# Kernel tuning notes

Hardware: AMD Instinct MI355X
Metric: run time of the kernel (lower is better)

Reference implementation:

```python
import jax, jax.numpy as jnp
import numpy as np

N = 100000
E = 1_600_000
IN_DIM = 128
HIDDEN = 128


def spmm(row, col, vals, H):
    # y[r] = sum_{edges e with row[e]==r} vals[e] * H[col[e]]
    msgs = vals[:, None] * H[col]          # [E, hidden] gather + scale
    return jax.ops.segment_sum(msgs, row, num_segments=H.shape[0])


def setup_inputs() -> dict:
    key = jax.random.key(0)
    ks = jax.random.split(key, 10)
    X = jax.random.normal(ks[0], (N, IN_DIM), dtype=jnp.float32)
    row = jax.random.randint(ks[1], (E,), 0, N, dtype=jnp.int32)
    col = jax.random.randint(ks[2], (E,), 0, N, dtype=jnp.int32)
    vals = jax.random.uniform(ks[3], (E,), dtype=jnp.float32)
    s_in = 1.0 / np.sqrt(IN_DIM)
    s_h = 1.0 / np.sqrt(HIDDEN)
    W_in = jax.random.normal(ks[4], (IN_DIM, HIDDEN), dtype=jnp.float32) * s_in
    b_in = jax.random.normal(ks[5], (HIDDEN,), dtype=jnp.float32) * s_in
    W_mp1 = jax.random.normal(ks[6], (HIDDEN, HIDDEN), dtype=jnp.float32) * s_h
    W_mp2 = jax.random.normal(ks[7], (HIDDEN, HIDDEN), dtype=jnp.float32) * s_h
    W_out = jax.random.normal(ks[8], (HIDDEN, 1), dtype=jnp.float32) * s_h
    b_out = jax.random.normal(ks[9], (1,), dtype=jnp.float32) * s_h
    return {"X": X, "row": row, "col": col, "vals": vals,
            "W_in": W_in, "b_in": b_in, "W_mp1": W_mp1, "W_mp2": W_mp2,
            "W_out": W_out, "b_out": b_out}


def reference(X, row, col, vals, W_in, b_in, W_mp1, W_mp2, W_out, b_out):
    H = jax.nn.relu(X @ W_in + b_in)          # [N, hidden]
    AH = spmm(row, col, vals, H)              # 1-hop propagation
    A2H = spmm(row, col, vals, AH)            # 2-hop propagation
    H2 = jax.nn.relu(AH @ W_mp1 + A2H @ W_mp2)
    return H2 @ W_out + b_out                 # [N, 1]
```

## Files before the change

### kernel.cpp

```cpp
#include <hip/hip_runtime.h>

#define N_NODES 100000
#define N_EDGES 1600000
#define NBUCK 391
#define NCHUNK 256
#define CHUNK 6250
#define LROW 136
#define DCAP 5120

typedef float f32x4 __attribute__((ext_vector_type(4)));
typedef _Float16 f16x8 __attribute__((ext_vector_type(8)));
typedef _Float16 h16x2 __attribute__((ext_vector_type(2)));

__device__ __forceinline__ unsigned f2h_bits(float f) {
    union { _Float16 h; unsigned short s; } c;
    c.h = (_Float16)f;
    return c.s;
}
__device__ __forceinline__ h16x2 u2h(unsigned u) {
    union { unsigned u; h16x2 h; } c;
    c.u = u;
    return c.h;
}
__device__ __forceinline__ unsigned pk16lo(unsigned hi, unsigned lo) {
    return __builtin_amdgcn_perm(hi, lo, 0x05040100u);
}
__device__ __forceinline__ unsigned pk16hi(unsigned hi, unsigned lo) {
    return __builtin_amdgcn_perm(hi, lo, 0x07060302u);
}
__device__ __forceinline__ float fdot2(h16x2 a, h16x2 b, float c) {
#if __has_builtin(__builtin_amdgcn_fdot2)
    return __builtin_amdgcn_fdot2(a, b, c, false);
#else
    return c + (float)a[0] * (float)b[0] + (float)a[1] * (float)b[1];
#endif
}

__device__ __forceinline__ f16x8 pack_h8(float4 a, float4 b) {
    f16x8 r;
    r[0] = (_Float16)a.x; r[1] = (_Float16)a.y;
    r[2] = (_Float16)a.z; r[3] = (_Float16)a.w;
    r[4] = (_Float16)b.x; r[5] = (_Float16)b.y;
    r[6] = (_Float16)b.z; r[7] = (_Float16)b.w;
    return r;
}


__global__ __launch_bounds__(256) void k_prep(const int* __restrict__ row,
                                              int* __restrict__ hmat,
                                              const float* __restrict__ Wa,
                                              const float* __restrict__ Wb,
                                              const float* __restrict__ Wc,
                                              unsigned short* __restrict__ Wta,
                                              unsigned short* __restrict__ Wtb,
                                              unsigned short* __restrict__ Wtc) {
    if (blockIdx.x < NCHUNK) {
        __shared__ int h[NBUCK];
        for (int i = threadIdx.x; i < NBUCK; i += 256) h[i] = 0;
        __syncthreads();
        int s = blockIdx.x * CHUNK, e = s + CHUNK;
        for (int i = s + threadIdx.x; i < e; i += 256)
            atomicAdd(&h[row[i] >> 8], 1);
        __syncthreads();
        for (int b = threadIdx.x; b < NBUCK; b += 256)
            hmat[blockIdx.x * NBUCK + b] = h[b];
    } else {
        int t = (blockIdx.x - NCHUNK) * 256 + threadIdx.x;
        int which = t >> 14;
        int i = t & 16383;
        int n = i & 127, k = i >> 7;
        const float* W = which == 0 ? Wa : which == 1 ? Wb : Wc;
        unsigned short* Wt = which == 0 ? Wta : which == 1 ? Wtb : Wtc;
        Wt[n * 128 + k] = (unsigned short)f2h_bits(W[k * 128 + n]);
    }
}

__global__ __launch_bounds__(512) void k_colscanB(const int* __restrict__ hmat,
                                                  int* __restrict__ bases,
                                                  int* __restrict__ bstart) {
    __shared__ int s[512];
    int b = blockIdx.x, t = threadIdx.x;
    if (b < NBUCK) {
        int v = (t < NCHUNK) ? hmat[t * NBUCK + b] : 0;
        s[t] = v;
        __syncthreads();
        for (int off = 1; off < 512; off <<= 1) {
            int x = (t >= off) ? s[t - off] : 0;
            __syncthreads();
            s[t] += x;
            __syncthreads();
        }
        if (t < NCHUNK) bases[t * NBUCK + b] = s[t] - v;
    } else {
        int v = 0;
        if (t < NBUCK) {
            for (int blk = 0; blk < NCHUNK; blk++) v += hmat[blk * NBUCK + t];
        }
        s[t] = v;
        __syncthreads();
        for (int off = 1; off < 512; off <<= 1) {
            int x = (t >= off) ? s[t - off] : 0;
            __syncthreads();
            s[t] += x;
            __syncthreads();
        }
        if (t < NBUCK) bstart[t] = s[t] - v;
        if (t == NBUCK) bstart[NBUCK] = N_EDGES;
    }
}

__global__ __launch_bounds__(256) void k_binC_gemm(const int* __restrict__ row,
                                                   const int* __restrict__ col,
                                                   const float* __restrict__ vals,
                                                   const int* __restrict__ bstart,
                                                   const int* __restrict__ bases,
                                                   int2* __restrict__ grouped,
                                                   const float* __restrict__ X,
                                                   const unsigned short* __restrict__ Wt,
                                                   const float* __restrict__ bvec,
                                                   unsigned short* __restrict__ H) {
    __shared__ __align__(16) char smraw[64 * LROW * 2];
    if (blockIdx.x < NCHUNK) {
        int* cnt = (int*)smraw;
        int* basl = (int*)(smraw + 1600);
        for (int i = threadIdx.x; i < NBUCK; i += 256) {
            cnt[i] = 0;
            basl[i] = bstart[i] + bases[blockIdx.x * NBUCK + i];
        }
        __syncthreads();
        int s = blockIdx.x * CHUNK, e = s + CHUNK;
        for (int i = s + threadIdx.x; i < e; i += 256) {
            int r = row[i];
            int b = r >> 8;
            int rank = atomicAdd(&cnt[b], 1);
            int pos = basl[b] + rank;
            unsigned hv = f2h_bits(vals[i]);
            grouped[pos] = make_int2(col[i], ((r & 255) << 14) | hv);
        }
    } else {
        unsigned short* lds = (unsigned short*)smraw;
        int tid = threadIdx.x;
        int lane = tid & 63, wv = tid >> 6;
        int quad = lane >> 4, c16 = lane & 15;

        f16x8 wf[2][4];
        float bb[2];
#pragma unroll
        for (int nt = 0; nt < 2; nt++) {
            int ng = wv * 2 + nt;
            bb[nt] = bvec[ng * 16 + c16];
#pragma unroll
            for (int kc = 0; kc < 4; kc++)
                wf[nt][kc] = *(const f16x8*)&Wt[(ng * 16 + c16) * 128 + kc * 32 + quad * 8];
        }

        int tilebase = (blockIdx.x - NCHUNK) * 64;
        const float4* Xg = (const float4*)X;
#pragma unroll
        for (int i = 0; i < 4; i++) {
            int c = tid + i * 256;
            int r = c >> 4, o = c & 15;
            int grow = tilebase + r;
            float4 f0 = make_float4(0.f, 0.f, 0.f, 0.f), f1 = f0;
            if (grow < N_NODES) {
                f0 = Xg[(size_t)grow * 32 + o * 2];
                f1 = Xg[(size_t)grow * 32 + o * 2 + 1];
            }
            *(f16x8*)&lds[r * LROW + o * 8] = pack_h8(f0, f1);
        }
        __syncthreads();

        f32x4 acc[4][2] = {};
#pragma unroll
        for (int t4 = 0; t4 < 4; t4++) {
#pragma unroll
            for (int kc = 0; kc < 4; kc++) {
                f16x8 af = *(const f16x8*)&lds[(t4 * 16 + c16) * LROW + kc * 32 + quad * 8];
#pragma unroll
                for (int nt = 0; nt < 2; nt++)
                    acc[t4][nt] = __builtin_amdgcn_mfma_f32_16x16x32_f16(af, wf[nt][kc],
                                                                        acc[t4][nt], 0, 0, 0);
            }
        }
        __syncthreads();

#pragma unroll
        for (int t4 = 0; t4 < 4; t4++)
#pragma unroll
            for (int nt = 0; nt < 2; nt++) {
                int ncol = (wv * 2 + nt) * 16 + c16;
#pragma unroll
                for (int r = 0; r < 4; r++) {
                    float v = fmaxf(acc[t4][nt][r] + bb[nt], 0.f);
                    lds[(t4 * 16 + quad * 4 + r) * LROW + ncol] = (unsigned short)f2h_bits(v);
                }
            }
        __syncthreads();
#pragma unroll
        for (int i = 0; i < 4; i++) {
            int c = tid + i * 256;
            int r = c >> 4, o = c & 15;
            int grow = tilebase + r;
            if (grow < N_NODES)
                *(uint4*)&H[(size_t)grow * 128 + o * 8] = *(const uint4*)&lds[r * LROW + o * 8];
        }
    }
}

__global__ __launch_bounds__(512) void k_binD(const int2* __restrict__ grouped,
                                              const int* __restrict__ bstart,
                                              unsigned* __restrict__ evf,
                                              int* __restrict__ row_ptr) {
    __shared__ int h[256], sc[256], cur[256];
    __shared__ int2 ebuf[DCAP];
    int b = blockIdx.x, t = threadIdx.x;
    int s0 = bstart[b], e0 = bstart[b + 1];
    int n = e0 - s0;
    bool inlds = (n <= DCAP);
    if (t < 256) h[t] = 0;
    __syncthreads();
    if (inlds) {
        for (int i = t; i < n; i += 512) ebuf[i] = grouped[s0 + i];
        __syncthreads();
        for (int i = t; i < n; i += 512)
            atomicAdd(&h[(ebuf[i].y >> 14) & 255], 1);
    } else {
        for (int i = s0 + t; i < e0; i += 512)
            atomicAdd(&h[(grouped[i].y >> 14) & 255], 1);
    }
    __syncthreads();
    int v = 0;
    if (t < 256) {
        v = h[t];
        sc[t] = v;
    }
    __syncthreads();
    for (int off = 1; off < 256; off <<= 1) {
        int x = (t >= off && t < 256) ? sc[t - off] : 0;
        __syncthreads();
        if (t < 256) sc[t] += x;
        __syncthreads();
    }
    if (t < 256) {
        int excl = sc[t] - v;
        cur[t] = excl;
        int grow = b * 256 + t;
        if (grow <= N_NODES) row_ptr[grow] = s0 + excl;
    }
    __syncthreads();
    if (inlds) {
        for (int i = t; i < n; i += 512) {
            int2 g = ebuf[i];
            int rl = (g.y >> 14) & 255;
            int p = atomicAdd(&cur[rl], 1);
            evf[s0 + p] = ((unsigned)g.x << 14) | (unsigned)(g.y & 0x3fff);
        }
    } else {
        for (int i = s0 + t; i < e0; i += 512) {
            int2 g = grouped[i];
            int rl = (g.y >> 14) & 255;
            int p = atomicAdd(&cur[rl], 1);
            evf[s0 + p] = ((unsigned)g.x << 14) | (unsigned)(g.y & 0x3fff);
        }
    }
}

__global__ __launch_bounds__(256) void k_spmm(const int* __restrict__ rp,
                                              const unsigned* __restrict__ evf,
                                              const unsigned* __restrict__ Hin,
                                              unsigned* __restrict__ Ho) {
    int tid = threadIdx.x;
    int lane = tid & 63;
    int q = lane >> 4, l16 = lane & 15;
    int wid = (blockIdx.x * 256 + tid) >> 6;
    int r0 = wid * 4 + q;
    int s = rp[r0];
    int e = rp[r0 + 1];
    float a0 = 0.f, a1 = 0.f, a2 = 0.f, a3 = 0.f;
    float a4 = 0.f, a5 = 0.f, a6 = 0.f, a7 = 0.f;
    for (int base = s; base < e; base += 16) {
        int cnt = e - base;
        if (cnt > 16) cnt = 16;
        unsigned ev = evf[base + (l16 < cnt ? l16 : cnt - 1)];
        for (int i = 0; i < cnt; i += 4) {
            int i1 = i + 1, i2 = i + 2, i3 = i + 3;
            unsigned u0 = __shfl(ev, (q << 4) + i, 64);
            unsigned u1 = __shfl(ev, (q << 4) + (i1 < cnt ? i1 : cnt - 1), 64);
            unsigned u2 = __shfl(ev, (q << 4) + (i2 < cnt ? i2 : cnt - 1), 64);
            unsigned u3 = __shfl(ev, (q << 4) + (i3 < cnt ? i3 : cnt - 1), 64);
            const uint4 h0 = *(const uint4*)&Hin[(size_t)(u0 >> 14) * 64 + l16 * 4];
            const uint4 h1 = *(const uint4*)&Hin[(size_t)(u1 >> 14) * 64 + l16 * 4];
            const uint4 h2 = *(const uint4*)&Hin[(size_t)(u2 >> 14) * 64 + l16 * 4];
            const uint4 h3 = *(const uint4*)&Hin[(size_t)(u3 >> 14) * 64 + l16 * 4];
            unsigned m0 = u0 & 0x3fffu;
            unsigned m1 = (i1 < cnt) ? (u1 & 0x3fffu) : 0u;
            unsigned m2 = (i2 < cnt) ? (u2 & 0x3fffu) : 0u;
            unsigned m3 = (i3 < cnt) ? (u3 & 0x3fffu) : 0u;
            h16x2 v01 = u2h(pk16lo(m1, m0));
            h16x2 v23 = u2h(pk16lo(m3, m2));
            a0 = fdot2(v01, u2h(pk16lo(h1.x, h0.x)), a0);
            a0 = fdot2(v23, u2h(pk16lo(h3.x, h2.x)), a0);
            a1 = fdot2(v01, u2h(pk16hi(h1.x, h0.x)), a1);
            a1 = fdot2(v23, u2h(pk16hi(h3.x, h2.x)), a1);
            a2 = fdot2(v01, u2h(pk16lo(h1.y, h0.y)), a2);
            a2 = fdot2(v23, u2h(pk16lo(h3.y, h2.y)), a2);
            a3 = fdot2(v01, u2h(pk16hi(h1.y, h0.y)), a3);
            a3 = fdot2(v23, u2h(pk16hi(h3.y, h2.y)), a3);
            a4 = fdot2(v01, u2h(pk16lo(h1.z, h0.z)), a4);
            a4 = fdot2(v23, u2h(pk16lo(h3.z, h2.z)), a4);
            a5 = fdot2(v01, u2h(pk16hi(h1.z, h0.z)), a5);
            a5 = fdot2(v23, u2h(pk16hi(h3.z, h2.z)), a5);
            a6 = fdot2(v01, u2h(pk16lo(h1.w, h0.w)), a6);
            a6 = fdot2(v23, u2h(pk16lo(h3.w, h2.w)), a6);
            a7 = fdot2(v01, u2h(pk16hi(h1.w, h0.w)), a7);
            a7 = fdot2(v23, u2h(pk16hi(h3.w, h2.w)), a7);
        }
    }
    uint4 p;
    p.x = (f2h_bits(a1) << 16) | f2h_bits(a0);
    p.y = (f2h_bits(a3) << 16) | f2h_bits(a2);
    p.z = (f2h_bits(a5) << 16) | f2h_bits(a4);
    p.w = (f2h_bits(a7) << 16) | f2h_bits(a6);
    *(uint4*)&Ho[(size_t)r0 * 64 + l16 * 4] = p;
}

__global__ __launch_bounds__(256) void k_gemm_out(const unsigned short* __restrict__ AH,
                                                  const unsigned short* __restrict__ A2H,
                                                  const unsigned short* __restrict__ Wt1,
                                                  const unsigned short* __restrict__ Wt2,
                                                  const float* __restrict__ Wout,
                                                  const float* __restrict__ bout,
                                                  float* __restrict__ out) {
    __shared__ unsigned short lds[2][64 * LROW];
    __shared__ float part[4][64];
    int tid = threadIdx.x;
    int lane = tid & 63, wv = tid >> 6;
    int quad = lane >> 4, c16 = lane & 15;

    f16x8 w1f[2][4], w2f[2][4];
    float wo[2];
#pragma unroll
    for (int nt = 0; nt < 2; nt++) {
        int ng = wv * 2 + nt;
        wo[nt] = Wout[ng * 16 + c16];
#pragma unroll
        for (int kc = 0; kc < 4; kc++) {
            w1f[nt][kc] = *(const f16x8*)&Wt1[(ng * 16 + c16) * 128 + kc * 32 + quad * 8];
            w2f[nt][kc] = *(const f16x8*)&Wt2[(ng * 16 + c16) * 128 + kc * 32 + quad * 8];
        }
    }
    float bo = bout[0];

    int tilebase = blockIdx.x * 64;
    const uint4* Ag = (const uint4*)(AH + (size_t)tilebase * 128);
    const uint4* Bg = (const uint4*)(A2H + (size_t)tilebase * 128);
#pragma unroll
    for (int i = 0; i < 4; i++) {
        int c = tid + i * 256;
        int r = c >> 4, o = c & 15;
        *(uint4*)&lds[0][r * LROW + o * 8] = Ag[c];
        *(uint4*)&lds[1][r * LROW + o * 8] = Bg[c];
    }
    __syncthreads();

    f32x4 acc[4][2] = {};
#pragma unroll
    for (int t4 = 0; t4 < 4; t4++) {
#pragma unroll
        for (int kc = 0; kc < 4; kc++) {
            f16x8 afA = *(const f16x8*)&lds[0][(t4 * 16 + c16) * LROW + kc * 32 + quad * 8];
            f16x8 afB = *(const f16x8*)&lds[1][(t4 * 16 + c16) * LROW + kc * 32 + quad * 8];
#pragma unroll
            for (int nt = 0; nt < 2; nt++) {
                acc[t4][nt] = __builtin_amdgcn_mfma_f32_16x16x32_f16(afA, w1f[nt][kc],
                                                                    acc[t4][nt], 0, 0, 0);
                acc[t4][nt] = __builtin_amdgcn_mfma_f32_16x16x32_f16(afB, w2f[nt][kc],
                                                                    acc[t4][nt], 0, 0, 0);
            }
        }
    }

#pragma unroll
    for (int t4 = 0; t4 < 4; t4++) {
        float p[4];
#pragma unroll
        for (int r = 0; r < 4; r++)
            p[r] = fmaxf(acc[t4][0][r], 0.f) * wo[0] + fmaxf(acc[t4][1][r], 0.f) * wo[1];
#pragma unroll
        for (int m = 1; m < 16; m <<= 1)
#pragma unroll
            for (int r = 0; r < 4; r++) p[r] += __shfl_xor(p[r], m, 64);
        if (c16 == 0)
#pragma unroll
            for (int r = 0; r < 4; r++) part[wv][t4 * 16 + quad * 4 + r] = p[r];
    }
    __syncthreads();
    if (tid < 64) {
        int orow = tilebase + tid;
        if (orow < N_NODES)
            out[orow] = part[0][tid] + part[1][tid] + part[2][tid] + part[3][tid] + bo;
    }
}


extern "C" void kernel_launch(void* const* d_in, const int* in_sizes, int n_in,
                              void* d_out, int out_size, void* d_ws, size_t ws_size,
                              hipStream_t stream) {
    const float* X    = (const float*)d_in[0];
    const int*   row  = (const int*)d_in[1];
    const int*   col  = (const int*)d_in[2];
    const float* vals = (const float*)d_in[3];
    const float* W_in = (const float*)d_in[4];
    const float* b_in = (const float*)d_in[5];
    const float* W1   = (const float*)d_in[6];
    const float* W2   = (const float*)d_in[7];
    const float* Wout = (const float*)d_in[8];
    const float* bout = (const float*)d_in[9];
    float* out = (float*)d_out;

    char* ws = (char*)d_ws;
    size_t off = 0;
    auto alloc = [&](size_t bytes) -> void* {
        void* p = ws + off;
        off += (bytes + 511) & ~(size_t)511;
        return p;
    };
    unsigned short* Hb  = (unsigned short*)alloc((size_t)N_NODES * 128 * 2);
    unsigned short* AHb = (unsigned short*)alloc((size_t)N_NODES * 128 * 2);
    unsigned short* A2b = (unsigned short*)alloc((size_t)N_NODES * 128 * 2);
    unsigned* evf  = (unsigned*)alloc((size_t)N_EDGES * 4);
    int2* grouped  = (int2*)alloc((size_t)N_EDGES * 8);
    unsigned short* Wtin = (unsigned short*)alloc(128 * 128 * 2);
    unsigned short* Wt1  = (unsigned short*)alloc(128 * 128 * 2);
    unsigned short* Wt2  = (unsigned short*)alloc(128 * 128 * 2);
    int*   hmat    = (int*)alloc((size_t)NCHUNK * NBUCK * 4);
    int*   bases   = (int*)alloc((size_t)NCHUNK * NBUCK * 4);
    int*   bstart  = (int*)alloc(512 * 4);
    int*   row_ptr = (int*)alloc((size_t)(N_NODES + 256) * 4);

    int gblk = (N_NODES + 63) / 64;

    k_prep<<<NCHUNK + 192, 256, 0, stream>>>(row, hmat, W_in, W1, W2, Wtin, Wt1, Wt2);
    k_colscanB<<<NBUCK + 1, 512, 0, stream>>>(hmat, bases, bstart);
    k_binC_gemm<<<NCHUNK + gblk, 256, 0, stream>>>(row, col, vals, bstart, bases,
                                                   grouped, X, Wtin, b_in, Hb);
    k_binD<<<NBUCK, 512, 0, stream>>>(grouped, bstart, evf, row_ptr);

    int sblk = N_NODES / 16;
    k_spmm<<<sblk, 256, 0, stream>>>(row_ptr, evf, (const unsigned*)Hb, (unsigned*)AHb);
    k_spmm<<<sblk, 256, 0, stream>>>(row_ptr, evf, (const unsigned*)AHb, (unsigned*)A2b);

    k_gemm_out<<<gblk, 256, 0, stream>>>(AHb, A2b, Wt1, Wt2, Wout, bout, out);
}
```

Baseline: 313.1 us.

## Split each SpMM row's edges across wave quarters and reduce with shuffles

The SpMM kernel now gives each 64-lane wave two rows instead of four. All four 16-lane quarters work on different edges of the same row, and the partial sums are combined at the end with xor shuffles. Edge fetches are wave-uniform 64-edge batches, and masked lanes get zero weights instead of per-iteration clamping. The aim is to cut the divergence and idle lanes that come from varying row degrees and to expose more independent gathers per wave. In exchange it launches twice as many blocks, adds a cross-lane reduction, and doubles accumulator registers.

Result: no change. 307.0 us (-2.0%).

```diff
diff --git a/kernel.cpp b/kernel.cpp
--- a/kernel.cpp
+++ b/kernel.cpp
@@ -265,6 +265,36 @@
     }
 }
 
+#define STEP16(EV, R, A0, A1, A2, A3, A4, A5, A6, A7)                          \
+    do {                                                                       \
+        unsigned u0 = __shfl(EV, (R) + q, 64);                                 \
+        unsigned u1 = __shfl(EV, (R) + 4 + q, 64);                             \
+        unsigned u2 = __shfl(EV, (R) + 8 + q, 64);                             \
+        unsigned u3 = __shfl(EV, (R) + 12 + q, 64);                            \
+        const uint4 h0 = *(const uint4*)&Hin[(size_t)(u0 >> 14) * 64 + l16 * 4]; \
+        const uint4 h1 = *(const uint4*)&Hin[(size_t)(u1 >> 14) * 64 + l16 * 4]; \
+        const uint4 h2 = *(const uint4*)&Hin[(size_t)(u2 >> 14) * 64 + l16 * 4]; \
+        const uint4 h3 = *(const uint4*)&Hin[(size_t)(u3 >> 14) * 64 + l16 * 4]; \
+        h16x2 v01 = u2h(pk16lo(u1 & 0x3fffu, u0 & 0x3fffu));                   \
+        h16x2 v23 = u2h(pk16lo(u3 & 0x3fffu, u2 & 0x3fffu));                   \
+        A0 = fdot2(v01, u2h(pk16lo(h1.x, h0.x)), A0);                          \
+        A0 = fdot2(v23, u2h(pk16lo(h3.x, h2.x)), A0);                          \
+        A1 = fdot2(v01, u2h(pk16hi(h1.x, h0.x)), A1);                          \
+        A1 = fdot2(v23, u2h(pk16hi(h3.x, h2.x)), A1);                          \
+        A2 = fdot2(v01, u2h(pk16lo(h1.y, h0.y)), A2);                          \
+        A2 = fdot2(v23, u2h(pk16lo(h3.y, h2.y)), A2);                          \
+        A3 = fdot2(v01, u2h(pk16hi(h1.y, h0.y)), A3);                          \
+        A3 = fdot2(v23, u2h(pk16hi(h3.y, h2.y)), A3);                          \
+        A4 = fdot2(v01, u2h(pk16lo(h1.z, h0.z)), A4);                          \
+        A4 = fdot2(v23, u2h(pk16lo(h3.z, h2.z)), A4);                          \
+        A5 = fdot2(v01, u2h(pk16hi(h1.z, h0.z)), A5);                          \
+        A5 = fdot2(v23, u2h(pk16hi(h3.z, h2.z)), A5);                          \
+        A6 = fdot2(v01, u2h(pk16lo(h1.w, h0.w)), A6);                          \
+        A6 = fdot2(v23, u2h(pk16lo(h3.w, h2.w)), A6);                          \
+        A7 = fdot2(v01, u2h(pk16hi(h1.w, h0.w)), A7);                          \
+        A7 = fdot2(v23, u2h(pk16hi(h3.w, h2.w)), A7);                          \
+    } while (0)
+
 __global__ __launch_bounds__(256) void k_spmm(const int* __restrict__ rp,
                                               const unsigned* __restrict__ evf,
                                               const unsigned* __restrict__ Hin,
@@ -273,55 +303,68 @@
     int lane = tid & 63;
     int q = lane >> 4, l16 = lane & 15;
     int wid = (blockIdx.x * 256 + tid) >> 6;
-    int r0 = wid * 4 + q;
-    int s = rp[r0];
-    int e = rp[r0 + 1];
-    float a0 = 0.f, a1 = 0.f, a2 = 0.f, a3 = 0.f;
-    float a4 = 0.f, a5 = 0.f, a6 = 0.f, a7 = 0.f;
-    for (int base = s; base < e; base += 16) {
-        int cnt = e - base;
-        if (cnt > 16) cnt = 16;
-        unsigned ev = evf[base + (l16 < cnt ? l16 : cnt - 1)];
-        for (int i = 0; i < cnt; i += 4) {
-            int i1 = i + 1, i2 = i + 2, i3 = i + 3;
-            unsigned u0 = __shfl(ev, (q << 4) + i, 64);
-            unsigned u1 = __shfl(ev, (q << 4) + (i1 < cnt ? i1 : cnt - 1), 64);
-            unsigned u2 = __shfl(ev, (q << 4) + (i2 < cnt ? i2 : cnt - 1), 64);
-            unsigned u3 = __shfl(ev, (q << 4) + (i3 < cnt ? i3 : cnt - 1), 64);
-            const uint4 h0 = *(const uint4*)&Hin[(size_t)(u0 >> 14) * 64 + l16 * 4];
-            const uint4 h1 = *(const uint4*)&Hin[(size_t)(u1 >> 14) * 64 + l16 * 4];
-            const uint4 h2 = *(const uint4*)&Hin[(size_t)(u2 >> 14) * 64 + l16 * 4];
-            const uint4 h3 = *(const uint4*)&Hin[(size_t)(u3 >> 14) * 64 + l16 * 4];
-            unsigned m0 = u0 & 0x3fffu;
-            unsigned m1 = (i1 < cnt) ? (u1 & 0x3fffu) : 0u;
-            unsigned m2 = (i2 < cnt) ? (u2 & 0x3fffu) : 0u;
-            unsigned m3 = (i3 < cnt) ? (u3 & 0x3fffu) : 0u;
-            h16x2 v01 = u2h(pk16lo(m1, m0));
-            h16x2 v23 = u2h(pk16lo(m3, m2));
-            a0 = fdot2(v01, u2h(pk16lo(h1.x, h0.x)), a0);
-            a0 = fdot2(v23, u2h(pk16lo(h3.x, h2.x)), a0);
-            a1 = fdot2(v01, u2h(pk16hi(h1.x, h0.x)), a1);
-            a1 = fdot2(v23, u2h(pk16hi(h3.x, h2.x)), a1);
-            a2 = fdot2(v01, u2h(pk16lo(h1.y, h0.y)), a2);
-            a2 = fdot2(v23, u2h(pk16lo(h3.y, h2.y)), a2);
-            a3 = fdot2(v01, u2h(pk16hi(h1.y, h0.y)), a3);
-            a3 = fdot2(v23, u2h(pk16hi(h3.y, h2.y)), a3);
-            a4 = fdot2(v01, u2h(pk16lo(h1.z, h0.z)), a4);
-            a4 = fdot2(v23, u2h(pk16lo(h3.z, h2.z)), a4);
-            a5 = fdot2(v01, u2h(pk16hi(h1.z, h0.z)), a5);
-            a5 = fdot2(v23, u2h(pk16hi(h3.z, h2.z)), a5);
-            a6 = fdot2(v01, u2h(pk16lo(h1.w, h0.w)), a6);
-            a6 = fdot2(v23, u2h(pk16lo(h3.w, h2.w)), a6);
-            a7 = fdot2(v01, u2h(pk16hi(h1.w, h0.w)), a7);
-            a7 = fdot2(v23, u2h(pk16hi(h3.w, h2.w)), a7);
-        }
-    }
-    uint4 p;
-    p.x = (f2h_bits(a1) << 16) | f2h_bits(a0);
-    p.y = (f2h_bits(a3) << 16) | f2h_bits(a2);
-    p.z = (f2h_bits(a5) << 16) | f2h_bits(a4);
-    p.w = (f2h_bits(a7) << 16) | f2h_bits(a6);
-    *(uint4*)&Ho[(size_t)r0 * 64 + l16 * 4] = p;
+    int rA = wid * 2;
+    int sA = __builtin_amdgcn_readfirstlane(rp[rA]);
+    int eA = __builtin_amdgcn_readfirstlane(rp[rA + 1]);
+    int eB = __builtin_amdgcn_readfirstlane(rp[rA + 2]);
+    int sB = eA;
+    float aA0 = 0.f, aA1 = 0.f, aA2 = 0.f, aA3 = 0.f;
+    float aA4 = 0.f, aA5 = 0.f, aA6 = 0.f, aA7 = 0.f;
+    float aB0 = 0.f, aB1 = 0.f, aB2 = 0.f, aB3 = 0.f;
+    float aB4 = 0.f, aB5 = 0.f, aB6 = 0.f, aB7 = 0.f;
+    int baseA = sA, baseB = sB;
+    while (baseA < eA || baseB < eB) {
+        int cntA = eA - baseA;
+        if (cntA > 64) cntA = 64;
+        if (cntA < 0) cntA = 0;
+        int cntB = eB - baseB;
+        if (cntB > 64) cntB = 64;
+        if (cntB < 0) cntB = 0;
+        unsigned evA = 0u, evB = 0u;
+        if (cntA) {
+            evA = evf[baseA + (lane < cntA ? lane : cntA - 1)];
+            if (lane >= cntA) evA &= ~0x3fffu;
+        }
+        if (cntB) {
+            evB = evf[baseB + (lane < cntB ? lane : cntB - 1)];
+            if (lane >= cntB) evB &= ~0x3fffu;
+        }
+        int cm = cntA > cntB ? cntA : cntB;
+        for (int r = 0; r < cm; r += 16) {
+            if (r < cntA) STEP16(evA, r, aA0, aA1, aA2, aA3, aA4, aA5, aA6, aA7);
+            if (r < cntB) STEP16(evB, r, aB0, aB1, aB2, aB3, aB4, aB5, aB6, aB7);
+        }
+        baseA += cntA;
+        baseB += cntB;
+    }
+    aA0 += __shfl_xor(aA0, 16, 64); aA0 += __shfl_xor(aA0, 32, 64);
+    aA1 += __shfl_xor(aA1, 16, 64); aA1 += __shfl_xor(aA1, 32, 64);
+    aA2 += __shfl_xor(aA2, 16, 64); aA2 += __shfl_xor(aA2, 32, 64);
+    aA3 += __shfl_xor(aA3, 16, 64); aA3 += __shfl_xor(aA3, 32, 64);
+    aA4 += __shfl_xor(aA4, 16, 64); aA4 += __shfl_xor(aA4, 32, 64);
+    aA5 += __shfl_xor(aA5, 16, 64); aA5 += __shfl_xor(aA5, 32, 64);
+    aA6 += __shfl_xor(aA6, 16, 64); aA6 += __shfl_xor(aA6, 32, 64);
+    aA7 += __shfl_xor(aA7, 16, 64); aA7 += __shfl_xor(aA7, 32, 64);
+    aB0 += __shfl_xor(aB0, 16, 64); aB0 += __shfl_xor(aB0, 32, 64);
+    aB1 += __shfl_xor(aB1, 16, 64); aB1 += __shfl_xor(aB1, 32, 64);
+    aB2 += __shfl_xor(aB2, 16, 64); aB2 += __shfl_xor(aB2, 32, 64);
+    aB3 += __shfl_xor(aB3, 16, 64); aB3 += __shfl_xor(aB3, 32, 64);
+    aB4 += __shfl_xor(aB4, 16, 64); aB4 += __shfl_xor(aB4, 32, 64);
+    aB5 += __shfl_xor(aB5, 16, 64); aB5 += __shfl_xor(aB5, 32, 64);
+    aB6 += __shfl_xor(aB6, 16, 64); aB6 += __shfl_xor(aB6, 32, 64);
+    aB7 += __shfl_xor(aB7, 16, 64); aB7 += __shfl_xor(aB7, 32, 64);
+    if (q < 2) {
+        float r0 = q ? aB0 : aA0, r1 = q ? aB1 : aA1;
+        float r2 = q ? aB2 : aA2, r3 = q ? aB3 : aA3;
+        float r4 = q ? aB4 : aA4, r5 = q ? aB5 : aA5;
+        float r6 = q ? aB6 : aA6, r7 = q ? aB7 : aA7;
+        uint4 p;
+        p.x = (f2h_bits(r1) << 16) | f2h_bits(r0);
+        p.y = (f2h_bits(r3) << 16) | f2h_bits(r2);
+        p.z = (f2h_bits(r5) << 16) | f2h_bits(r4);
+        p.w = (f2h_bits(r7) << 16) | f2h_bits(r6);
+        *(uint4*)&Ho[(size_t)(rA + q) * 64 + l16 * 4] = p;
+    }
 }
 
 __global__ __launch_bounds__(256) void k_gemm_out(const unsigned short* __restrict__ AH,
@@ -446,7 +489,7 @@
                                                    grouped, X, Wtin, b_in, Hb);
     k_binD<<<NBUCK, 512, 0, stream>>>(grouped, bstart, evf, row_ptr);
 
-    int sblk = N_NODES / 16;
+    int sblk = N_NODES / 8;
     k_spmm<<<sblk, 256, 0, stream>>>(row_ptr, evf, (const unsigned*)Hb, (unsigned*)AHb);
     k_spmm<<<sblk, 256, 0, stream>>>(row_ptr, evf, (const unsigned*)AHb, (unsigned*)A2b);
 
```
